# Kernel optimization log

Hardware: AMD Instinct MI355X
Metric: run time of the kernel (lower is better)

The kernel has to match this reference:

```python
import jax, jax.numpy as jnp
import numpy as np

M, K, E, N, TOPK = 4096, 1024, 8, 1024, 2

def setup_inputs() -> dict:
    key = jax.random.key(0)
    k1, k2, k3, k4, k5 = jax.random.split(key, 5)
    hidden_states = jax.random.normal(k1, (M, K), dtype=jnp.float32)
    w1 = jax.random.normal(k2, (E, K, 2 * N), dtype=jnp.float32) * 0.02
    w2 = jax.random.normal(k3, (E, N, K), dtype=jnp.float32) * 0.02
    topk_weights = jax.random.uniform(k4, (M, TOPK), dtype=jnp.float32)
    topk_ids = jax.random.randint(k5, (M, TOPK), 0, E, dtype=jnp.int64)
    return {"hidden_states": hidden_states, "w1": w1, "w2": w2,
            "topk_weights": topk_weights, "topk_ids": topk_ids}

def reference(hidden_states, w1, w2, topk_weights, topk_ids):
    # Fused MoE: per expert e, y_e = silu_and_mul(x @ w1[e]) @ w2[e];
    # output[m] = sum_k topk_weights[m,k] * y_{topk_ids[m,k]}[m]
    num_experts = w1.shape[0]
    n = w2.shape[1]

    def expert_step(acc, inputs):
        w1_e, w2_e, e = inputs
        gate_up = hidden_states @ w1_e            # [M, 2N]
        gate, up = gate_up[:, :n], gate_up[:, n:]
        h = jax.nn.silu(gate) * up                 # [M, N]
        y_e = h @ w2_e                             # [M, K]
        # combined routing weight of expert e per token (scatter-free finalize)
        coef = jnp.sum(jnp.where(topk_ids == e, topk_weights, 0.0), axis=1)  # [M]
        return acc + coef[:, None] * y_e, None

    init = jnp.zeros_like(hidden_states)
    out, _ = jax.lax.scan(expert_step, init,
                          (w1, w2, jnp.arange(num_experts, dtype=topk_ids.dtype)))
    return out
```

## Files before the change

### kernel.cpp

```cpp
#include <hip/hip_runtime.h>


#define M_TOK   4096
#define K_DIM   1024
#define N_DIM   1024
#define E_NUM   8
#define NPAIR   8192
#define BM      128
#define ROWS_CAP 9216
#define NROWBLK 72
#define HBLK    32

typedef unsigned short u16;
typedef unsigned int   u32;
typedef __attribute__((ext_vector_type(8))) short bf16x8;
typedef __attribute__((ext_vector_type(4))) float f32x4;

#define GPTR(p) ((const __attribute__((address_space(1))) u32*)(const void*)(p))
#define LPTR(p) ((__attribute__((address_space(3))) u32*)(void*)(p))

__device__ __forceinline__ u16 f2bf(float f) {
  union { float f; u32 u; } v; v.f = f;
  u32 r = v.u + 0x7FFFu + ((v.u >> 16) & 1u);
  return (u16)(r >> 16);
}
__device__ __forceinline__ float bf2f(u16 u) {
  union { u32 u; float f; } v; v.u = ((u32)u) << 16;
  return v.f;
}

__global__ __launch_bounds__(256) void hist_kernel(
    const int* __restrict__ topk_ids, int* __restrict__ blockhist) {
  __shared__ int wcnt[4][E_NUM];
  const int t = threadIdx.x, wave = t >> 6, lane = t & 63;
  int e = topk_ids[blockIdx.x * 256 + t] & 7;
#pragma unroll
  for (int ee = 0; ee < E_NUM; ++ee) {
    unsigned long long m = __ballot(e == ee);
    if (lane == ee) wcnt[wave][ee] = (int)__popcll(m);
  }
  __syncthreads();
  if (t < E_NUM) {
    int s = wcnt[0][t] + wcnt[1][t] + wcnt[2][t] + wcnt[3][t];
    blockhist[blockIdx.x * E_NUM + t] = s;
  }
}

__global__ __launch_bounds__(256) void scan_kernel(
    const int* __restrict__ blockhist, int* __restrict__ baseoff,
    int* __restrict__ pair_token, int* __restrict__ block_expert) {
  __shared__ int cnt[E_NUM], off[E_NUM], pad[E_NUM];
  const int t = threadIdx.x;
  if (t < E_NUM) {
    int run = 0;
    for (int b = 0; b < HBLK; ++b) {
      baseoff[b * E_NUM + t] = run;
      run += blockhist[b * E_NUM + t];
    }
    cnt[t] = run;
  }
  __syncthreads();
  if (t == 0) {
    int run = 0, blk = 0;
    for (int e = 0; e < E_NUM; ++e) {
      off[e] = run;
      int padded = ((cnt[e] + BM - 1) / BM) * BM;
      pad[e] = padded;
      for (int b = 0; b < padded / BM; ++b) block_expert[blk++] = e;
      run += padded;
    }
    for (; blk < NROWBLK; ++blk) block_expert[blk] = -1;
  }
  __syncthreads();
  for (int i = t; i < HBLK * E_NUM; i += 256) baseoff[i] += off[i & 7];
  for (int e = 0; e < E_NUM; ++e) {
    int s = off[e] + cnt[e], epos = off[e] + pad[e];
    for (int r = s + t; r < epos; r += 256) pair_token[r] = 0;
  }
}

__global__ __launch_bounds__(256) void assign_kernel(
    const int* __restrict__ topk_ids, const int* __restrict__ baseoff,
    int* __restrict__ pair_token, int* __restrict__ pos_of) {
  __shared__ int wcnt[4][E_NUM], wbase[4][E_NUM];
  const int t = threadIdx.x, wave = t >> 6, lane = t & 63;
  const int p = blockIdx.x * 256 + t;
  const int e = topk_ids[p] & 7;
  int rank = 0;
#pragma unroll
  for (int ee = 0; ee < E_NUM; ++ee) {
    unsigned long long m = __ballot(e == ee);
    if (e == ee) rank = (int)__popcll(m & ((1ull << lane) - 1ull));
    if (lane == ee) wcnt[wave][ee] = (int)__popcll(m);
  }
  __syncthreads();
  if (t < E_NUM) {
    int run = baseoff[blockIdx.x * E_NUM + t];
    for (int w = 0; w < 4; ++w) { wbase[w][t] = run; run += wcnt[w][t]; }
  }
  __syncthreads();
  int pos = wbase[wave][e] + rank;
  pair_token[pos] = p >> 1;
  pos_of[p] = pos;
}

__global__ __launch_bounds__(256) void convert_kernel(
    const float* __restrict__ in, u16* __restrict__ out) {
  int i = blockIdx.x * 256 + threadIdx.x;
  float4 v = ((const float4*)in)[i];
  ushort4 o;
  o.x = f2bf(v.x); o.y = f2bf(v.y); o.z = f2bf(v.z); o.w = f2bf(v.w);
  ((ushort4*)out)[i] = o;
}

__global__ __launch_bounds__(256) void transpose_convert(
    const float* __restrict__ in, u16* __restrict__ out, int R, int Cc) {
  __shared__ float lds[64][65];
  const float* src = in + (size_t)blockIdx.z * R * Cc;
  u16* dst = out + (size_t)blockIdx.z * R * Cc;
  int r0 = blockIdx.x * 64, c0 = blockIdx.y * 64;
  int t = threadIdx.x;
#pragma unroll
  for (int it = 0; it < 16; ++it) {
    int lin = it * 256 + t;
    int rr = lin >> 6, cc = lin & 63;
    lds[cc][rr] = src[(size_t)(r0 + rr) * Cc + c0 + cc];
  }
  __syncthreads();
#pragma unroll
  for (int it = 0; it < 8; ++it) {
    int lin = it * 512 + t * 2;
    int cc = lin >> 6, rr = lin & 63;
    ushort2 o;
    o.x = f2bf(lds[cc][rr]);
    o.y = f2bf(lds[cc][rr + 1]);
    *(ushort2*)&dst[(size_t)(c0 + cc) * R + r0 + rr] = o;
  }
}

template <bool GATHER, int NB>
__global__ __launch_bounds__(256, NB == 2 ? 2 : 3) void gemm128(
    const u16* __restrict__ A, const u16* __restrict__ Bt, u16* __restrict__ Out,
    const int* __restrict__ pair_token, const int* __restrict__ block_expert) {
  const int bx = ((int)blockIdx.x & 7) * (NROWBLK / 8) + ((int)blockIdx.x >> 3);
  const int e = block_expert[bx];
  if (e < 0) return;
  __shared__ __align__(16) u16 As[128 * 64];
  __shared__ __align__(16) u16 Bs[NB * 128 * 64];
  const int tid = threadIdx.x;
  const int wave = tid >> 6;
  const int lane = tid & 63;
  const int wr = wave >> 1;
  const int wc = wave & 1;
  const int srow = wave * 8 + (lane >> 3);
  const int kc = ((lane & 7) ^ (srow & 7)) << 3;

  const u16* ap[4];
#pragma unroll
  for (int is = 0; is < 4; ++is) {
    int rt = is * 32 + srow;
    int grow = bx * BM + rt;
    int arow = GATHER ? pair_token[grow] : grow;
    ap[is] = A + (size_t)arow * K_DIM + kc;
  }
  const u16* bp[NB][4];
  const u16* base_e = Bt + (size_t)e * (NB * N_DIM) * K_DIM;
#pragma unroll
  for (int nb = 0; nb < NB; ++nb)
#pragma unroll
    for (int is = 0; is < 4; ++is) {
      int n = nb * N_DIM + blockIdx.y * 128 + is * 32 + srow;
      bp[nb][is] = base_e + (size_t)n * K_DIM + kc;
    }
  u16* alds = As + wave * 512;
  u16* blds = Bs + wave * 512;

  f32x4 acc[NB][4][4];
#pragma unroll
  for (int nb = 0; nb < NB; ++nb)
#pragma unroll
    for (int i = 0; i < 4; ++i)
#pragma unroll
      for (int j = 0; j < 4; ++j) acc[nb][i][j] = f32x4{0.f, 0.f, 0.f, 0.f};

  for (int k0 = 0; k0 < K_DIM; k0 += 64) {
#pragma unroll
    for (int is = 0; is < 4; ++is)
      __builtin_amdgcn_global_load_lds(GPTR(ap[is] + k0), LPTR(alds + is * 2048), 16, 0, 0);
#pragma unroll
    for (int nb = 0; nb < NB; ++nb)
#pragma unroll
      for (int is = 0; is < 4; ++is)
        __builtin_amdgcn_global_load_lds(GPTR(bp[nb][is] + k0), LPTR(blds + nb * 8192 + is * 2048), 16, 0, 0);
    __syncthreads();
#pragma unroll
    for (int ks = 0; ks < 2; ++ks) {
      const int cq = ks * 4 + (lane >> 4);
      bf16x8 af[4], bfr[NB][4];
#pragma unroll
      for (int i = 0; i < 4; ++i) {
        int row = wr * 64 + i * 16 + (lane & 15);
        af[i] = *(const bf16x8*)&As[row * 64 + ((cq ^ (row & 7)) << 3)];
      }
#pragma unroll
      for (int nb = 0; nb < NB; ++nb)
#pragma unroll
        for (int j = 0; j < 4; ++j) {
          int n = wc * 64 + j * 16 + (lane & 15);
          bfr[nb][j] = *(const bf16x8*)&Bs[nb * 8192 + n * 64 + ((cq ^ (n & 7)) << 3)];
        }
#pragma unroll
      for (int nb = 0; nb < NB; ++nb)
#pragma unroll
        for (int i = 0; i < 4; ++i)
#pragma unroll
          for (int j = 0; j < 4; ++j)
            acc[nb][i][j] = __builtin_amdgcn_mfma_f32_16x16x32_bf16(af[i], bfr[nb][j], acc[nb][i][j], 0, 0, 0);
    }
    __syncthreads();
  }

  const size_t rbase = (size_t)bx * BM + wr * 64 + ((lane >> 4) * 4);
  const int cbase = blockIdx.y * 128 + wc * 64 + (lane & 15);
#pragma unroll
  for (int i = 0; i < 4; ++i)
#pragma unroll
    for (int j = 0; j < 4; ++j)
#pragma unroll
      for (int r = 0; r < 4; ++r) {
        float v;
        if (NB == 2) {
          float g = acc[0][i][j][r], u = acc[1][i][j][r];
          v = g * u / (1.f + __expf(-g));
        } else {
          v = acc[0][i][j][r];
        }
        Out[(rbase + i * 16 + r) * N_DIM + cbase + j * 16] = f2bf(v);
      }
}

__global__ __launch_bounds__(256) void gather_kernel(
    const u16* __restrict__ y, const float* __restrict__ tw,
    const int* __restrict__ pos_of, float* __restrict__ out) {
  int m = blockIdx.x;
  int k = threadIdx.x * 4;
  int p0 = pos_of[m * 2 + 0], p1 = pos_of[m * 2 + 1];
  float w0 = tw[m * 2 + 0], w1 = tw[m * 2 + 1];
  ushort4 y0 = *(const ushort4*)&y[(size_t)p0 * 1024 + k];
  ushort4 y1 = *(const ushort4*)&y[(size_t)p1 * 1024 + k];
  float4 o;
  o.x = w0 * bf2f(y0.x) + w1 * bf2f(y1.x);
  o.y = w0 * bf2f(y0.y) + w1 * bf2f(y1.y);
  o.z = w0 * bf2f(y0.z) + w1 * bf2f(y1.z);
  o.w = w0 * bf2f(y0.w) + w1 * bf2f(y1.w);
  *(float4*)&out[(size_t)m * 1024 + k] = o;
}

extern "C" void kernel_launch(void* const* d_in, const int* in_sizes, int n_in,
                              void* d_out, int out_size, void* d_ws, size_t ws_size,
                              hipStream_t stream) {
  const float* hs = (const float*)d_in[0];
  const float* w1 = (const float*)d_in[1];
  const float* w2 = (const float*)d_in[2];
  const float* tw = (const float*)d_in[3];
  const int* tids = (const int*)d_in[4];
  float* out = (float*)d_out;

  char* ws = (char*)d_ws;
  u16* hsb = (u16*)(ws);
  u16* w1t = (u16*)(ws + (size_t)(8u << 20));
  u16* w2t = (u16*)(ws + (size_t)(40u << 20));
  u16* h   = (u16*)(ws + (size_t)(56u << 20));
  u16* y   = (u16*)(ws + (size_t)(76u << 20));
  int* pair_token   = (int*)(ws + (size_t)(96u << 20));
  int* pos_of       = (int*)(ws + (size_t)(96u << 20) + 64 * 1024);
  int* block_expert = (int*)(ws + (size_t)(96u << 20) + 128 * 1024);
  int* blockhist    = (int*)(ws + (size_t)(96u << 20) + 192 * 1024);
  int* baseoff      = (int*)(ws + (size_t)(96u << 20) + 256 * 1024);

  hist_kernel<<<HBLK, 256, 0, stream>>>(tids, blockhist);
  scan_kernel<<<1, 256, 0, stream>>>(blockhist, baseoff, pair_token, block_expert);
  assign_kernel<<<HBLK, 256, 0, stream>>>(tids, baseoff, pair_token, pos_of);
  convert_kernel<<<4096, 256, 0, stream>>>(hs, hsb);
  transpose_convert<<<dim3(16, 32, E_NUM), 256, 0, stream>>>(w1, w1t, 1024, 2048);
  transpose_convert<<<dim3(16, 16, E_NUM), 256, 0, stream>>>(w2, w2t, 1024, 1024);
  gemm128<true, 2><<<dim3(NROWBLK, 8), 256, 0, stream>>>(hsb, w1t, h, pair_token, block_expert);
  gemm128<false, 1><<<dim3(NROWBLK, 8), 256, 0, stream>>>(h, w2t, y, pair_token, block_expert);
  gather_kernel<<<4096, 256, 0, stream>>>(y, tw, pos_of, out);
}
```

Measured before the change: 251.8 us.

## Rewrite expert GEMMs as 8-wave multi-buffered pipelined kernels with phased MFMA

```diff
diff --git a/kernel.cpp b/kernel.cpp
--- a/kernel.cpp
+++ b/kernel.cpp
@@ -18,6 +18,7 @@
 
 #define GPTR(p) ((const __attribute__((address_space(1))) u32*)(const void*)(p))
 #define LPTR(p) ((__attribute__((address_space(3))) u32*)(void*)(p))
+#define MFMA_BF16 __builtin_amdgcn_mfma_f32_16x16x32_bf16
 
 __device__ __forceinline__ u16 f2bf(float f) {
   union { float f; u32 u; } v; v.f = f;
@@ -139,93 +140,201 @@
 }
 
 template <bool GATHER, int NB>
-__global__ __launch_bounds__(256, NB == 2 ? 2 : 3) void gemm128(
+__global__ __launch_bounds__(512, NB == 2 ? 1 : 4) void gemm8p(
     const u16* __restrict__ A, const u16* __restrict__ Bt, u16* __restrict__ Out,
     const int* __restrict__ pair_token, const int* __restrict__ block_expert) {
+  constexpr int NBUF = (NB == 2) ? 3 : 2;
+  constexpr int A_ELEMS = 128 * 64;
+  constexpr int B_ELEMS = NB * 128 * 64;
+  constexpr int KT = K_DIM / 64;
+  constexpr int DEPTH = (NB == 2) ? 2 : 1;
+
   const int bx = ((int)blockIdx.x & 7) * (NROWBLK / 8) + ((int)blockIdx.x >> 3);
   const int e = block_expert[bx];
   if (e < 0) return;
-  __shared__ __align__(16) u16 As[128 * 64];
-  __shared__ __align__(16) u16 Bs[NB * 128 * 64];
+  const int by = blockIdx.y;
+
+  extern __shared__ __align__(16) u16 smem[];
+  u16* As = smem;
+  u16* Bs = smem + NBUF * A_ELEMS;
+
   const int tid = threadIdx.x;
   const int wave = tid >> 6;
   const int lane = tid & 63;
-  const int wr = wave >> 1;
-  const int wc = wave & 1;
-  const int srow = wave * 8 + (lane >> 3);
-  const int kc = ((lane & 7) ^ (srow & 7)) << 3;
-
-  const u16* ap[4];
-#pragma unroll
-  for (int is = 0; is < 4; ++is) {
-    int rt = is * 32 + srow;
+  const int wr  = wave >> 2;
+  const int wcc = wave & 3;
+  const int sr8 = lane >> 3;
+  const int kc  = ((lane & 7) ^ sr8) << 3;
+
+  const u16* apg[2];
+#pragma unroll
+  for (int is = 0; is < 2; ++is) {
+    int rt = is * 64 + wave * 8 + sr8;
     int grow = bx * BM + rt;
     int arow = GATHER ? pair_token[grow] : grow;
-    ap[is] = A + (size_t)arow * K_DIM + kc;
-  }
-  const u16* bp[NB][4];
+    apg[is] = A + (size_t)arow * K_DIM + kc;
+  }
+  const u16* bpg[NB * 2];
   const u16* base_e = Bt + (size_t)e * (NB * N_DIM) * K_DIM;
 #pragma unroll
+  for (int is = 0; is < NB * 2; ++is) {
+    int rt = is * 64 + wave * 8 + sr8;
+    int nb = rt >> 7;
+    int n = nb * N_DIM + by * 128 + (rt & 127);
+    bpg[is] = base_e + (size_t)n * K_DIM + kc;
+  }
+
+#define STAGE_A(buf, is, koff) __builtin_amdgcn_global_load_lds( \
+    GPTR(apg[is] + (koff)), LPTR(&As[(buf) * A_ELEMS + (is) * 4096 + wave * 512]), 16, 0, 0)
+#define STAGE_B(buf, is, koff) __builtin_amdgcn_global_load_lds( \
+    GPTR(bpg[is] + (koff)), LPTR(&Bs[(buf) * B_ELEMS + (is) * 4096 + wave * 512]), 16, 0, 0)
+#define RDA(dst, base, i, ks) do { const int row_ = wr * 64 + (i) * 16 + (lane & 15); \
+    dst = *(const bf16x8*)&(base)[row_ * 64 + ((((ks) * 4 + (lane >> 4)) ^ (row_ & 7)) << 3)]; } while (0)
+#define RDB(dst, base, nbv, j, ks) do { const int n_ = (nbv) * 128 + wcc * 32 + (j) * 16 + (lane & 15); \
+    dst = *(const bf16x8*)&(base)[n_ * 64 + ((((ks) * 4 + (lane >> 4)) ^ (n_ & 7)) << 3)]; } while (0)
+#define PHASE_OPEN() do { __builtin_amdgcn_s_barrier(); \
+    asm volatile("s_waitcnt lgkmcnt(0)" ::: "memory"); \
+    __builtin_amdgcn_sched_barrier(0); \
+    __builtin_amdgcn_s_setprio(1); } while (0)
+#define PHASE_CLOSE() do { __builtin_amdgcn_s_setprio(0); \
+    __builtin_amdgcn_s_barrier(); } while (0)
+
+  f32x4 acc[NB][4][2];
+#pragma unroll
   for (int nb = 0; nb < NB; ++nb)
 #pragma unroll
-    for (int is = 0; is < 4; ++is) {
-      int n = nb * N_DIM + blockIdx.y * 128 + is * 32 + srow;
-      bp[nb][is] = base_e + (size_t)n * K_DIM + kc;
+    for (int i = 0; i < 4; ++i)
+#pragma unroll
+      for (int j = 0; j < 2; ++j) acc[nb][i][j] = f32x4{0.f, 0.f, 0.f, 0.f};
+
+  if constexpr (NB == 2) {
+    STAGE_A(0, 0, 0); STAGE_A(0, 1, 0);
+    STAGE_B(0, 0, 0); STAGE_B(0, 1, 0); STAGE_B(0, 2, 0); STAGE_B(0, 3, 0);
+    __builtin_amdgcn_sched_barrier(0);
+    STAGE_A(1, 0, 64); STAGE_A(1, 1, 64);
+    STAGE_B(1, 0, 64); STAGE_B(1, 1, 64); STAGE_B(1, 2, 64); STAGE_B(1, 3, 64);
+    __builtin_amdgcn_sched_barrier(0);
+    asm volatile("s_waitcnt vmcnt(6)" ::: "memory");
+  } else {
+    STAGE_A(0, 0, 0); STAGE_A(0, 1, 0);
+    STAGE_B(0, 0, 0); STAGE_B(0, 1, 0);
+    asm volatile("s_waitcnt vmcnt(0)" ::: "memory");
+  }
+  __builtin_amdgcn_s_barrier();
+
+  int cur = 0;
+  int nxt = DEPTH;
+  for (int t = 0; t < KT; ++t) {
+    const u16* Ab = &As[cur * A_ELEMS];
+    const u16* Bb = &Bs[cur * B_ELEMS];
+    const int koff = (t + DEPTH) * 64;
+    const bool issue = (t < KT - DEPTH);
+
+    if constexpr (NB == 2) {
+      bf16x8 bq[2][2];
+      {
+        bf16x8 af0, af1;
+        RDA(af0, Ab, 0, 0); RDA(af1, Ab, 1, 0);
+        RDB(bq[0][0], Bb, 0, 0, 0); RDB(bq[0][1], Bb, 0, 1, 0);
+        RDB(bq[1][0], Bb, 1, 0, 0); RDB(bq[1][1], Bb, 1, 1, 0);
+        if (issue) { STAGE_B(nxt, 0, koff); STAGE_B(nxt, 1, koff); }
+        PHASE_OPEN();
+#pragma unroll
+        for (int nb = 0; nb < 2; ++nb)
+#pragma unroll
+          for (int j = 0; j < 2; ++j) {
+            acc[nb][0][j] = MFMA_BF16(af0, bq[nb][j], acc[nb][0][j], 0, 0, 0);
+            acc[nb][1][j] = MFMA_BF16(af1, bq[nb][j], acc[nb][1][j], 0, 0, 0);
+          }
+        PHASE_CLOSE();
+      }
+      {
+        bf16x8 af2, af3;
+        RDA(af2, Ab, 2, 0); RDA(af3, Ab, 3, 0);
+        if (issue) { STAGE_B(nxt, 2, koff); STAGE_B(nxt, 3, koff); }
+        PHASE_OPEN();
+#pragma unroll
+        for (int nb = 0; nb < 2; ++nb)
+#pragma unroll
+          for (int j = 0; j < 2; ++j) {
+            acc[nb][2][j] = MFMA_BF16(af2, bq[nb][j], acc[nb][2][j], 0, 0, 0);
+            acc[nb][3][j] = MFMA_BF16(af3, bq[nb][j], acc[nb][3][j], 0, 0, 0);
+          }
+        PHASE_CLOSE();
+      }
+      {
+        bf16x8 af0, af1;
+        RDA(af0, Ab, 0, 1); RDA(af1, Ab, 1, 1);
+        RDB(bq[0][0], Bb, 0, 0, 1); RDB(bq[0][1], Bb, 0, 1, 1);
+        RDB(bq[1][0], Bb, 1, 0, 1); RDB(bq[1][1], Bb, 1, 1, 1);
+        if (issue) STAGE_A(nxt, 0, koff);
+        PHASE_OPEN();
+#pragma unroll
+        for (int nb = 0; nb < 2; ++nb)
+#pragma unroll
+          for (int j = 0; j < 2; ++j) {
+            acc[nb][0][j] = MFMA_BF16(af0, bq[nb][j], acc[nb][0][j], 0, 0, 0);
+            acc[nb][1][j] = MFMA_BF16(af1, bq[nb][j], acc[nb][1][j], 0, 0, 0);
+          }
+        PHASE_CLOSE();
+      }
+      {
+        bf16x8 af2, af3;
+        RDA(af2, Ab, 2, 1); RDA(af3, Ab, 3, 1);
+        if (issue) STAGE_A(nxt, 1, koff);
+        PHASE_OPEN();
+#pragma unroll
+        for (int nb = 0; nb < 2; ++nb)
+#pragma unroll
+          for (int j = 0; j < 2; ++j) {
+            acc[nb][2][j] = MFMA_BF16(af2, bq[nb][j], acc[nb][2][j], 0, 0, 0);
+            acc[nb][3][j] = MFMA_BF16(af3, bq[nb][j], acc[nb][3][j], 0, 0, 0);
+          }
+        __builtin_amdgcn_s_setprio(0);
+        if (t < KT - 2)       asm volatile("s_waitcnt vmcnt(6)" ::: "memory");
+        else if (t == KT - 2) asm volatile("s_waitcnt vmcnt(0)" ::: "memory");
+        __builtin_amdgcn_s_barrier();
+      }
+    } else {
+      {
+        bf16x8 af[4], bq[2];
+        RDA(af[0], Ab, 0, 0); RDA(af[1], Ab, 1, 0); RDA(af[2], Ab, 2, 0); RDA(af[3], Ab, 3, 0);
+        RDB(bq[0], Bb, 0, 0, 0); RDB(bq[1], Bb, 0, 1, 0);
+        if (issue) { STAGE_B(nxt, 0, koff); STAGE_A(nxt, 0, koff); }
+        PHASE_OPEN();
+#pragma unroll
+        for (int i = 0; i < 4; ++i)
+#pragma unroll
+          for (int j = 0; j < 2; ++j)
+            acc[0][i][j] = MFMA_BF16(af[i], bq[j], acc[0][i][j], 0, 0, 0);
+        PHASE_CLOSE();
+      }
+      {
+        bf16x8 af[4], bq[2];
+        RDA(af[0], Ab, 0, 1); RDA(af[1], Ab, 1, 1); RDA(af[2], Ab, 2, 1); RDA(af[3], Ab, 3, 1);
+        RDB(bq[0], Bb, 0, 0, 1); RDB(bq[1], Bb, 0, 1, 1);
+        if (issue) { STAGE_B(nxt, 1, koff); STAGE_A(nxt, 1, koff); }
+        PHASE_OPEN();
+#pragma unroll
+        for (int i = 0; i < 4; ++i)
+#pragma unroll
+          for (int j = 0; j < 2; ++j)
+            acc[0][i][j] = MFMA_BF16(af[i], bq[j], acc[0][i][j], 0, 0, 0);
+        __builtin_amdgcn_s_setprio(0);
+        if (t < KT - 1) asm volatile("s_waitcnt vmcnt(0)" ::: "memory");
+        __builtin_amdgcn_s_barrier();
+      }
     }
-  u16* alds = As + wave * 512;
-  u16* blds = Bs + wave * 512;
-
-  f32x4 acc[NB][4][4];
-#pragma unroll
-  for (int nb = 0; nb < NB; ++nb)
-#pragma unroll
-    for (int i = 0; i < 4; ++i)
-#pragma unroll
-      for (int j = 0; j < 4; ++j) acc[nb][i][j] = f32x4{0.f, 0.f, 0.f, 0.f};
-
-  for (int k0 = 0; k0 < K_DIM; k0 += 64) {
-#pragma unroll
-    for (int is = 0; is < 4; ++is)
-      __builtin_amdgcn_global_load_lds(GPTR(ap[is] + k0), LPTR(alds + is * 2048), 16, 0, 0);
-#pragma unroll
-    for (int nb = 0; nb < NB; ++nb)
-#pragma unroll
-      for (int is = 0; is < 4; ++is)
-        __builtin_amdgcn_global_load_lds(GPTR(bp[nb][is] + k0), LPTR(blds + nb * 8192 + is * 2048), 16, 0, 0);
-    __syncthreads();
-#pragma unroll
-    for (int ks = 0; ks < 2; ++ks) {
-      const int cq = ks * 4 + (lane >> 4);
-      bf16x8 af[4], bfr[NB][4];
-#pragma unroll
-      for (int i = 0; i < 4; ++i) {
-        int row = wr * 64 + i * 16 + (lane & 15);
-        af[i] = *(const bf16x8*)&As[row * 64 + ((cq ^ (row & 7)) << 3)];
-      }
-#pragma unroll
-      for (int nb = 0; nb < NB; ++nb)
-#pragma unroll
-        for (int j = 0; j < 4; ++j) {
-          int n = wc * 64 + j * 16 + (lane & 15);
-          bfr[nb][j] = *(const bf16x8*)&Bs[nb * 8192 + n * 64 + ((cq ^ (n & 7)) << 3)];
-        }
-#pragma unroll
-      for (int nb = 0; nb < NB; ++nb)
-#pragma unroll
-        for (int i = 0; i < 4; ++i)
-#pragma unroll
-          for (int j = 0; j < 4; ++j)
-            acc[nb][i][j] = __builtin_amdgcn_mfma_f32_16x16x32_bf16(af[i], bfr[nb][j], acc[nb][i][j], 0, 0, 0);
-    }
-    __syncthreads();
+    cur = (cur == NBUF - 1) ? 0 : cur + 1;
+    nxt = (nxt == NBUF - 1) ? 0 : nxt + 1;
   }
 
   const size_t rbase = (size_t)bx * BM + wr * 64 + ((lane >> 4) * 4);
-  const int cbase = blockIdx.y * 128 + wc * 64 + (lane & 15);
+  const int cbase = by * 128 + wcc * 32 + (lane & 15);
 #pragma unroll
   for (int i = 0; i < 4; ++i)
 #pragma unroll
-    for (int j = 0; j < 4; ++j)
+    for (int j = 0; j < 2; ++j)
 #pragma unroll
       for (int r = 0; r < 4; ++r) {
         float v;
@@ -237,6 +346,12 @@
         }
         Out[(rbase + i * 16 + r) * N_DIM + cbase + j * 16] = f2bf(v);
       }
+#undef STAGE_A
+#undef STAGE_B
+#undef RDA
+#undef RDB
+#undef PHASE_OPEN
+#undef PHASE_CLOSE
 }
 
 __global__ __launch_bounds__(256) void gather_kernel(
@@ -284,7 +399,9 @@
   convert_kernel<<<4096, 256, 0, stream>>>(hs, hsb);
   transpose_convert<<<dim3(16, 32, E_NUM), 256, 0, stream>>>(w1, w1t, 1024, 2048);
   transpose_convert<<<dim3(16, 16, E_NUM), 256, 0, stream>>>(w2, w2t, 1024, 1024);
-  gemm128<true, 2><<<dim3(NROWBLK, 8), 256, 0, stream>>>(hsb, w1t, h, pair_token, block_expert);
-  gemm128<false, 1><<<dim3(NROWBLK, 8), 256, 0, stream>>>(h, w2t, y, pair_token, block_expert);
+  size_t lds1 = (size_t)3 * (128 * 64 + 2 * 128 * 64) * sizeof(u16);
+  size_t lds2 = (size_t)2 * (128 * 64 + 1 * 128 * 64) * sizeof(u16);
+  gemm8p<true, 2><<<dim3(NROWBLK, 8), 512, lds1, stream>>>(hsb, w1t, h, pair_token, block_expert);
+  gemm8p<false, 1><<<dim3(NROWBLK, 8), 512, lds2, stream>>>(h, w2t, y, pair_token, block_expert);
   gather_kernel<<<4096, 256, 0, stream>>>(y, tw, pos_of, out);
 }
```

After: 263.9 us. 1.05x slower.

## Fuse routing, activation conversion and weight transposes into one prep kernel

Applied to the files above, without the earlier changes.

```diff
diff --git a/kernel.cpp b/kernel.cpp
--- a/kernel.cpp
+++ b/kernel.cpp
@@ -9,7 +9,6 @@
 #define BM      128
 #define ROWS_CAP 9216
 #define NROWBLK 72
-#define HBLK    32
 
 typedef unsigned short u16;
 typedef unsigned int   u32;
@@ -29,112 +28,104 @@
   return v.f;
 }
 
-__global__ __launch_bounds__(256) void hist_kernel(
-    const int* __restrict__ topk_ids, int* __restrict__ blockhist) {
-  __shared__ int wcnt[4][E_NUM];
-  const int t = threadIdx.x, wave = t >> 6, lane = t & 63;
-  int e = topk_ids[blockIdx.x * 256 + t] & 7;
-#pragma unroll
-  for (int ee = 0; ee < E_NUM; ++ee) {
-    unsigned long long m = __ballot(e == ee);
-    if (lane == ee) wcnt[wave][ee] = (int)__popcll(m);
+__device__ __forceinline__ void transpose_tile64(
+    const float* __restrict__ src, u16* __restrict__ dst, int R, int Cc,
+    int rb, int cb, void* shm) {
+  float* lds = (float*)shm;
+  const int r0 = rb * 64, c0 = cb * 64;
+  const int t = threadIdx.x;
+#pragma unroll
+  for (int it = 0; it < 4; ++it) {
+    int lin = it * 256 + t;
+    int rr = lin >> 4, c4 = (lin & 15) << 2;
+    float4 v = *(const float4*)&src[(size_t)(r0 + rr) * Cc + c0 + c4];
+    lds[rr * 67 + c4 + 0] = v.x; lds[rr * 67 + c4 + 1] = v.y;
+    lds[rr * 67 + c4 + 2] = v.z; lds[rr * 67 + c4 + 3] = v.w;
   }
   __syncthreads();
-  if (t < E_NUM) {
-    int s = wcnt[0][t] + wcnt[1][t] + wcnt[2][t] + wcnt[3][t];
-    blockhist[blockIdx.x * E_NUM + t] = s;
-  }
-}
-
-__global__ __launch_bounds__(256) void scan_kernel(
-    const int* __restrict__ blockhist, int* __restrict__ baseoff,
-    int* __restrict__ pair_token, int* __restrict__ block_expert) {
-  __shared__ int cnt[E_NUM], off[E_NUM], pad[E_NUM];
+#pragma unroll
+  for (int it = 0; it < 4; ++it) {
+    int lin = it * 256 + t;
+    int cc = lin >> 4, r4 = (lin & 15) << 2;
+    ushort4 o;
+    o.x = f2bf(lds[(r4 + 0) * 67 + cc]);
+    o.y = f2bf(lds[(r4 + 1) * 67 + cc]);
+    o.z = f2bf(lds[(r4 + 2) * 67 + cc]);
+    o.w = f2bf(lds[(r4 + 3) * 67 + cc]);
+    *(ushort4*)&dst[(size_t)(c0 + cc) * R + r0 + r4] = o;
+  }
+}
+
+__global__ __launch_bounds__(256) void prep_route_kernel(
+    const float* __restrict__ hs, const float* __restrict__ w1,
+    const float* __restrict__ w2, const int* __restrict__ topk_ids,
+    u16* __restrict__ hsb, u16* __restrict__ w1t, u16* __restrict__ w2t,
+    int* __restrict__ pair_token, int* __restrict__ pos_of,
+    int* __restrict__ block_expert) {
+  __shared__ __align__(16) char shm[17408];
+  const int bid = blockIdx.x;
   const int t = threadIdx.x;
-  if (t < E_NUM) {
-    int run = 0;
-    for (int b = 0; b < HBLK; ++b) {
-      baseoff[b * E_NUM + t] = run;
-      run += blockhist[b * E_NUM + t];
-    }
-    cnt[t] = run;
-  }
-  __syncthreads();
-  if (t == 0) {
-    int run = 0, blk = 0;
+  if (bid == 0) {
+    int* lcnt = (int*)shm;
+    __shared__ int cnt[E_NUM], off[E_NUM], pad[E_NUM];
+    int c[E_NUM];
+#pragma unroll
+    for (int e = 0; e < E_NUM; ++e) c[e] = 0;
+    for (int i = 0; i < 32; ++i) c[topk_ids[t * 32 + i] & 7]++;
+#pragma unroll
+    for (int e = 0; e < E_NUM; ++e) lcnt[t * 8 + e] = c[e];
+    __syncthreads();
+    if (t < E_NUM) {
+      int run = 0;
+      for (int i = 0; i < 256; ++i) {
+        int v = lcnt[i * 8 + t]; lcnt[i * 8 + t] = run; run += v;
+      }
+      cnt[t] = run;
+    }
+    __syncthreads();
+    if (t == 0) {
+      int run = 0, blk = 0;
+      for (int e = 0; e < E_NUM; ++e) {
+        off[e] = run;
+        int padded = ((cnt[e] + BM - 1) / BM) * BM;
+        pad[e] = padded;
+        for (int b = 0; b < padded / BM; ++b) block_expert[blk++] = e;
+        run += padded;
+      }
+      for (; blk < NROWBLK; ++blk) block_expert[blk] = -1;
+    }
+    __syncthreads();
+    for (int i = 0; i < 32; ++i) {
+      int p = t * 32 + i;
+      int e = topk_ids[p] & 7;
+      int idx = t * 8 + e;
+      int pos = off[e] + lcnt[idx];
+      lcnt[idx] = lcnt[idx] + 1;
+      pair_token[pos] = p >> 1;
+      pos_of[p] = pos;
+    }
     for (int e = 0; e < E_NUM; ++e) {
-      off[e] = run;
-      int padded = ((cnt[e] + BM - 1) / BM) * BM;
-      pad[e] = padded;
-      for (int b = 0; b < padded / BM; ++b) block_expert[blk++] = e;
-      run += padded;
-    }
-    for (; blk < NROWBLK; ++blk) block_expert[blk] = -1;
-  }
-  __syncthreads();
-  for (int i = t; i < HBLK * E_NUM; i += 256) baseoff[i] += off[i & 7];
-  for (int e = 0; e < E_NUM; ++e) {
-    int s = off[e] + cnt[e], epos = off[e] + pad[e];
-    for (int r = s + t; r < epos; r += 256) pair_token[r] = 0;
-  }
-}
-
-__global__ __launch_bounds__(256) void assign_kernel(
-    const int* __restrict__ topk_ids, const int* __restrict__ baseoff,
-    int* __restrict__ pair_token, int* __restrict__ pos_of) {
-  __shared__ int wcnt[4][E_NUM], wbase[4][E_NUM];
-  const int t = threadIdx.x, wave = t >> 6, lane = t & 63;
-  const int p = blockIdx.x * 256 + t;
-  const int e = topk_ids[p] & 7;
-  int rank = 0;
-#pragma unroll
-  for (int ee = 0; ee < E_NUM; ++ee) {
-    unsigned long long m = __ballot(e == ee);
-    if (e == ee) rank = (int)__popcll(m & ((1ull << lane) - 1ull));
-    if (lane == ee) wcnt[wave][ee] = (int)__popcll(m);
-  }
-  __syncthreads();
-  if (t < E_NUM) {
-    int run = baseoff[blockIdx.x * E_NUM + t];
-    for (int w = 0; w < 4; ++w) { wbase[w][t] = run; run += wcnt[w][t]; }
-  }
-  __syncthreads();
-  int pos = wbase[wave][e] + rank;
-  pair_token[pos] = p >> 1;
-  pos_of[p] = pos;
-}
-
-__global__ __launch_bounds__(256) void convert_kernel(
-    const float* __restrict__ in, u16* __restrict__ out) {
-  int i = blockIdx.x * 256 + threadIdx.x;
-  float4 v = ((const float4*)in)[i];
-  ushort4 o;
-  o.x = f2bf(v.x); o.y = f2bf(v.y); o.z = f2bf(v.z); o.w = f2bf(v.w);
-  ((ushort4*)out)[i] = o;
-}
-
-__global__ __launch_bounds__(256) void transpose_convert(
-    const float* __restrict__ in, u16* __restrict__ out, int R, int Cc) {
-  __shared__ float lds[64][65];
-  const float* src = in + (size_t)blockIdx.z * R * Cc;
-  u16* dst = out + (size_t)blockIdx.z * R * Cc;
-  int r0 = blockIdx.x * 64, c0 = blockIdx.y * 64;
-  int t = threadIdx.x;
-#pragma unroll
-  for (int it = 0; it < 16; ++it) {
-    int lin = it * 256 + t;
-    int rr = lin >> 6, cc = lin & 63;
-    lds[cc][rr] = src[(size_t)(r0 + rr) * Cc + c0 + cc];
-  }
-  __syncthreads();
-#pragma unroll
-  for (int it = 0; it < 8; ++it) {
-    int lin = it * 512 + t * 2;
-    int cc = lin >> 6, rr = lin & 63;
-    ushort2 o;
-    o.x = f2bf(lds[cc][rr]);
-    o.y = f2bf(lds[cc][rr + 1]);
-    *(ushort2*)&dst[(size_t)(c0 + cc) * R + r0 + rr] = o;
+      int s = off[e] + cnt[e], epos = off[e] + pad[e];
+      for (int r = s + t; r < epos; r += 256) pair_token[r] = 0;
+    }
+  } else if (bid <= 4096) {
+    int i = (bid - 1) * 256 + t;
+    float4 v = ((const float4*)hs)[i];
+    ushort4 o;
+    o.x = f2bf(v.x); o.y = f2bf(v.y); o.z = f2bf(v.z); o.w = f2bf(v.w);
+    ((ushort4*)hsb)[i] = o;
+  } else if (bid <= 8192) {
+    int idx = bid - 4097;
+    int e = idx >> 9, rem = idx & 511;
+    int cb = rem >> 4, rb = rem & 15;
+    transpose_tile64(w1 + (size_t)e * 1024 * 2048, w1t + (size_t)e * 1024 * 2048,
+                     1024, 2048, rb, cb, shm);
+  } else {
+    int idx = bid - 8193;
+    int e = idx >> 8, rem = idx & 255;
+    int cb = rem >> 4, rb = rem & 15;
+    transpose_tile64(w2 + (size_t)e * 1024 * 1024, w2t + (size_t)e * 1024 * 1024,
+                     1024, 1024, rb, cb, shm);
   }
 }
 
@@ -275,15 +266,9 @@
   int* pair_token   = (int*)(ws + (size_t)(96u << 20));
   int* pos_of       = (int*)(ws + (size_t)(96u << 20) + 64 * 1024);
   int* block_expert = (int*)(ws + (size_t)(96u << 20) + 128 * 1024);
-  int* blockhist    = (int*)(ws + (size_t)(96u << 20) + 192 * 1024);
-  int* baseoff      = (int*)(ws + (size_t)(96u << 20) + 256 * 1024);
-
-  hist_kernel<<<HBLK, 256, 0, stream>>>(tids, blockhist);
-  scan_kernel<<<1, 256, 0, stream>>>(blockhist, baseoff, pair_token, block_expert);
-  assign_kernel<<<HBLK, 256, 0, stream>>>(tids, baseoff, pair_token, pos_of);
-  convert_kernel<<<4096, 256, 0, stream>>>(hs, hsb);
-  transpose_convert<<<dim3(16, 32, E_NUM), 256, 0, stream>>>(w1, w1t, 1024, 2048);
-  transpose_convert<<<dim3(16, 16, E_NUM), 256, 0, stream>>>(w2, w2t, 1024, 1024);
+
+  prep_route_kernel<<<10241, 256, 0, stream>>>(
+      hs, w1, w2, tids, hsb, w1t, w2t, pair_token, pos_of, block_expert);
   gemm128<true, 2><<<dim3(NROWBLK, 8), 256, 0, stream>>>(hsb, w1t, h, pair_token, block_expert);
   gemm128<false, 1><<<dim3(NROWBLK, 8), 256, 0, stream>>>(h, w2t, y, pair_token, block_expert);
   gather_kernel<<<4096, 256, 0, stream>>>(y, tw, pos_of, out);
```

Measured after the change: 237.1 us (median of 3 runs). -5.9%, faster.
